# Kernel tuning notes

Measured on AMD Instinct MI355X. Metric: run time of the kernel, lower is better.

The kernel has to match this reference:

```python
import jax, jax.numpy as jnp
import numpy as np

EMBED_DIM = 1024
SEQ_LEN = 2048
BATCH = 8


def setup_inputs() -> dict:
    key = jax.random.key(0)
    ks = jax.random.split(key, 7)
    s = 1.0 / np.sqrt(EMBED_DIM)
    x = jax.random.normal(ks[0], (BATCH, SEQ_LEN, EMBED_DIM), dtype=jnp.float32)
    # torch nn.Linear stores weight as [out, in]; init U(-1/sqrt(in), 1/sqrt(in))
    Wq = jax.random.uniform(ks[1], (EMBED_DIM, EMBED_DIM), jnp.float32, -s, s)
    bq = jax.random.uniform(ks[2], (EMBED_DIM,), jnp.float32, -s, s)
    Wk = jax.random.uniform(ks[3], (EMBED_DIM, EMBED_DIM), jnp.float32, -s, s)
    bk = jax.random.uniform(ks[4], (EMBED_DIM,), jnp.float32, -s, s)
    Wv = jax.random.uniform(ks[5], (EMBED_DIM, EMBED_DIM), jnp.float32, -s, s)
    bv = jax.random.uniform(ks[6], (EMBED_DIM,), jnp.float32, -s, s)
    return {"x": x, "Wq": Wq, "bq": bq, "Wk": Wk, "bk": bk, "Wv": Wv, "bv": bv}


def reference(x, Wq, bq, Wk, bk, Wv, bv):
    # Linear projections (torch Linear: x @ W.T + b)
    q = jnp.einsum("bse,oe->bso", x, Wq) + bq
    k = jnp.einsum("bse,oe->bso", x, Wk) + bk
    v = jnp.einsum("bse,oe->bso", x, Wv) + bv
    scale = 1.0 / jnp.sqrt(jnp.float32(EMBED_DIM))
    sims = jnp.einsum("bqe,bke->bqk", q, k) * scale  # [B, S, S]
    causal = jnp.tril(jnp.ones((SEQ_LEN, SEQ_LEN), dtype=bool))
    masked = jnp.where(causal, sims, jnp.float32(-1e9))
    attn = jax.nn.softmax(masked, axis=2)
    return jnp.einsum("bqk,bke->bqe", attn, v)
```

## Files before the change

kernel.cpp:

```cpp
#include <hip/hip_runtime.h>
#include <hip/hip_bf16.h>
#include <stdint.h>
#include <math.h>

#define DEVI __device__ __forceinline__

typedef __attribute__((ext_vector_type(8))) __bf16    bf16x8;
typedef __attribute__((ext_vector_type(8))) _Float16  f16x8;
typedef __attribute__((ext_vector_type(4))) float     f32x4;

constexpr int BM = 128, BN = 128, BK = 64;

DEVI unsigned int pack2(float a, float b) {
  unsigned short ha = __builtin_bit_cast(unsigned short, __float2bfloat16(a));
  unsigned short hb = __builtin_bit_cast(unsigned short, __float2bfloat16(b));
  return (unsigned int)ha | ((unsigned int)hb << 16);
}

__global__ __launch_bounds__(256) void k_cvt_all(const float* __restrict__ x,
                                                 const float* __restrict__ Wq,
                                                 const float* __restrict__ Wk,
                                                 const float* __restrict__ Wv,
                                                 __hip_bfloat16* __restrict__ xb,
                                                 __hip_bfloat16* __restrict__ Wqb,
                                                 __hip_bfloat16* __restrict__ Wkb,
                                                 __hip_bfloat16* __restrict__ Wvb) {
  int i = blockIdx.x * 256 + threadIdx.x;
  const float* src;
  __hip_bfloat16* dst;
  int k;
  if (i < 4194304) {
    src = x; dst = xb; k = i;
  } else {
    int j = i - 4194304;
    int w = j >> 18;
    k = j & 262143;
    src = (w == 0) ? Wq : (w == 1) ? Wk : Wv;
    dst = (w == 0) ? Wqb : (w == 1) ? Wkb : Wvb;
  }
  float4 f = ((const float4*)src)[k];
  uint2 u;
  u.x = pack2(f.x, f.y);
  u.y = pack2(f.z, f.w);
  ((uint2*)dst)[k] = u;
}

DEVI void stage_tile(const __hip_bfloat16* gbase, int ld, unsigned short* lds, int tid) {
#pragma unroll
  for (int j = 0; j < 4; ++j) {
    int g   = j * 256 + tid;
    int row = g >> 3;
    int cp  = g & 7;
    int c   = cp ^ (row & 7);
    const __hip_bfloat16* src = gbase + (size_t)row * ld + c * 8;
    unsigned short* dst = lds + (size_t)(j * 256 + (tid & ~63)) * 8;
    __builtin_amdgcn_global_load_lds((__attribute__((address_space(1))) void*)(src),
                                     (__attribute__((address_space(3))) void*)(dst),
                                     16, 0, 0);
  }
}

DEVI bf16x8 read_frag(const unsigned short* lds, int row, int kcol) {
  int c  = kcol >> 3;
  int cp = c ^ (row & 7);
  return *(const bf16x8*)(lds + row * 64 + cp * 8);
}

DEVI void gemm_core(const __hip_bfloat16* A0, int lda,
                    const __hip_bfloat16* B0, int ldb,
                    int ktiles, f32x4 (&acc)[4][4]) {
  __shared__ unsigned short sA[BM * BK];
  __shared__ unsigned short sB[BN * BK];
  const int tid  = threadIdx.x;
  const int lane = tid & 63;
  const int wid  = tid >> 6;
  const int quad = lane >> 4;
  const int lr   = lane & 15;
  const int wm   = (wid >> 1) * 64;
  const int wn   = (wid & 1) * 64;
  const f32x4 Z = {0.f, 0.f, 0.f, 0.f};
#pragma unroll
  for (int i = 0; i < 4; ++i)
#pragma unroll
    for (int j = 0; j < 4; ++j) acc[i][j] = Z;

  for (int kt = 0; kt < ktiles; ++kt) {
    stage_tile(A0 + kt * BK, lda, sA, tid);
    stage_tile(B0 + kt * BK, ldb, sB, tid);
    __syncthreads();
#pragma unroll
    for (int ks = 0; ks < BK; ks += 32) {
      bf16x8 af[4], bfr[4];
#pragma unroll
      for (int t = 0; t < 4; ++t) af[t]  = read_frag(sA, wm + t * 16 + lr, ks + quad * 8);
#pragma unroll
      for (int t = 0; t < 4; ++t) bfr[t] = read_frag(sB, wn + t * 16 + lr, ks + quad * 8);
#pragma unroll
      for (int i = 0; i < 4; ++i)
#pragma unroll
        for (int j = 0; j < 4; ++j)
          acc[i][j] = __builtin_amdgcn_mfma_f32_16x16x32_bf16(af[i], bfr[j], acc[i][j], 0, 0, 0);
    }
    __syncthreads();
  }
}

__global__ __launch_bounds__(256, 4) void k_proj_qkv(const __hip_bfloat16* __restrict__ X,
                                                     const __hip_bfloat16* __restrict__ Wq,
                                                     const __hip_bfloat16* __restrict__ Wk,
                                                     const __hip_bfloat16* __restrict__ Wv,
                                                     const float* __restrict__ bq,
                                                     const float* __restrict__ bk,
                                                     const float* __restrict__ bv,
                                                     __hip_bfloat16* __restrict__ Q,
                                                     __hip_bfloat16* __restrict__ Kp,
                                                     __hip_bfloat16* __restrict__ Vt) {
  const int id = blockIdx.x;
  const int w  = id >> 10;
  const int i2 = id & 1023;
  const int mt = ((i2 & 7) << 4) | ((i2 >> 3) & 15);
  const int nt = i2 >> 7;
  const int m0 = mt * BM;
  const int n0 = nt * BN;

  const __hip_bfloat16* W = (w == 0) ? Wq : (w == 1) ? Wk : Wv;
  const float* bias       = (w == 0) ? bq : (w == 1) ? bk : bv;

  f32x4 acc[4][4];
  gemm_core(X + (size_t)m0 * 1024, 1024, W + (size_t)n0 * 1024, 1024, 16, acc);

  const int tid = threadIdx.x, lane = tid & 63, wid = tid >> 6;
  const int quad = lane >> 4, lr = lane & 15;
  const int wm = (wid >> 1) * 64, wn = (wid & 1) * 64;
  float bvv[4];
#pragma unroll
  for (int j = 0; j < 4; ++j) bvv[j] = bias[n0 + wn + j * 16 + lr];

  if (w != 2) {
    __hip_bfloat16* C = (w == 0) ? Q : Kp;
#pragma unroll
    for (int i = 0; i < 4; ++i)
#pragma unroll
      for (int j = 0; j < 4; ++j) {
        int n = n0 + wn + j * 16 + lr;
#pragma unroll
        for (int r = 0; r < 4; ++r) {
          int m = m0 + wm + i * 16 + quad * 4 + r;
          C[(size_t)m * 1024 + n] = __float2bfloat16(acc[i][j][r] + bvv[j]);
        }
      }
  } else {
    const int b = m0 >> 11;
    __hip_bfloat16* Cb = Vt + ((size_t)b << 21);
    const int sb = (m0 & 2047) + wm;
#pragma unroll
    for (int i = 0; i < 4; ++i)
#pragma unroll
      for (int j = 0; j < 4; ++j) {
        int n  = n0 + wn + j * 16 + lr;
        int s0 = sb + i * 16 + quad * 4;
        uint2 u;
        u.x = pack2(acc[i][j][0] + bvv[j], acc[i][j][1] + bvv[j]);
        u.y = pack2(acc[i][j][2] + bvv[j], acc[i][j][3] + bvv[j]);
        *(uint2*)(Cb + (size_t)n * 2048 + s0) = u;
      }
  }
}

__global__ __launch_bounds__(256, 4) void k_scores(const __hip_bfloat16* __restrict__ Q,
                                                   const __hip_bfloat16* __restrict__ Kmat,
                                                   _Float16* __restrict__ S, int b0) {
  const int id = blockIdx.x;
  const int z = id & 3;
  const int b = b0 + z;
  const int i = id >> 2;
  int qt = (int)((sqrtf(8.f * (float)i + 1.f) - 1.f) * 0.5f);
  while ((qt + 1) * (qt + 2) / 2 <= i) ++qt;
  while (qt * (qt + 1) / 2 > i) --qt;
  const int kt = i - qt * (qt + 1) / 2;

  const int m0 = qt * BM, n0 = kt * BN;
  f32x4 acc[4][4];
  const __hip_bfloat16* A0 = Q    + ((size_t)b << 21) + (size_t)m0 * 1024;
  const __hip_bfloat16* B0 = Kmat + ((size_t)b << 21) + (size_t)n0 * 1024;
  gemm_core(A0, 1024, B0, 1024, 16, acc);

  _Float16* Sb = S + ((size_t)z << 22);
  const int tid = threadIdx.x, lane = tid & 63, wid = tid >> 6;
  const int quad = lane >> 4, lr = lane & 15;
  const int wm = (wid >> 1) * 64, wn = (wid & 1) * 64;
#pragma unroll
  for (int i2 = 0; i2 < 4; ++i2)
#pragma unroll
    for (int j = 0; j < 4; ++j) {
      int n = n0 + wn + j * 16 + lr;
#pragma unroll
      for (int r = 0; r < 4; ++r) {
        int m = m0 + wm + i2 * 16 + quad * 4 + r;
        Sb[(size_t)m * 2048 + n] = (_Float16)(acc[i2][j][r] * 0.03125f);
      }
    }
}

__global__ __launch_bounds__(256) void k_softmax(_Float16* __restrict__ S) {
  const int row = blockIdx.x;
  const int q = row & 2047;
  _Float16* srow = S + ((size_t)row << 11);
  const int t = threadIdx.x;
  const int k0 = t << 3;

  f16x8 h = ((const f16x8*)srow)[t];
  float v[8];
  float mx = -1e30f;
#pragma unroll
  for (int i = 0; i < 8; ++i) {
    float f = (float)h[i];
    v[i] = (k0 + i <= q) ? f : -1e30f;
    mx = fmaxf(mx, v[i]);
  }
#pragma unroll
  for (int off = 32; off > 0; off >>= 1) mx = fmaxf(mx, __shfl_xor(mx, off));
  __shared__ float rmax[4], rsum[4];
  if ((t & 63) == 0) rmax[t >> 6] = mx;
  __syncthreads();
  mx = fmaxf(fmaxf(rmax[0], rmax[1]), fmaxf(rmax[2], rmax[3]));

  float e[8], s = 0.f;
#pragma unroll
  for (int i = 0; i < 8; ++i) { e[i] = __expf(v[i] - mx); s += e[i]; }
#pragma unroll
  for (int off = 32; off > 0; off >>= 1) s += __shfl_xor(s, off);
  if ((t & 63) == 0) rsum[t >> 6] = s;
  __syncthreads();
  s = rsum[0] + rsum[1] + rsum[2] + rsum[3];
  const float inv = 1.0f / s;

  bf16x8 o;
#pragma unroll
  for (int i = 0; i < 8; ++i) o[i] = (__bf16)(e[i] * inv);
  ((bf16x8*)srow)[t] = o;
}

__global__ __launch_bounds__(256, 4) void k_pv(const _Float16* __restrict__ Sbase,
                                               const __hip_bfloat16* __restrict__ Vt,
                                               float* __restrict__ out, int b0) {
  const int id = blockIdx.x;
  const int z = id & 3;
  const int b = b0 + z;
  const int r2 = id >> 2;
  const int nt = r2 & 7;
  const int qt = 15 - (r2 >> 3);
  const int m0 = qt * BM, n0 = nt * BN;
  const __hip_bfloat16* P  = (const __hip_bfloat16*)(Sbase + ((size_t)z << 22));
  const __hip_bfloat16* A0 = P + (size_t)m0 * 2048;
  const __hip_bfloat16* B0 = Vt + ((size_t)b << 21) + (size_t)n0 * 2048;
  const int ktiles = 2 * qt + 2;
  f32x4 acc[4][4];
  gemm_core(A0, 2048, B0, 2048, ktiles, acc);

  float* Cb = out + ((size_t)b << 21);
  const int tid = threadIdx.x, lane = tid & 63, wid = tid >> 6;
  const int quad = lane >> 4, lr = lane & 15;
  const int wm = (wid >> 1) * 64, wn = (wid & 1) * 64;
#pragma unroll
  for (int i = 0; i < 4; ++i)
#pragma unroll
    for (int j = 0; j < 4; ++j) {
      int n = n0 + wn + j * 16 + lr;
#pragma unroll
      for (int r = 0; r < 4; ++r) {
        int m = m0 + wm + i * 16 + quad * 4 + r;
        Cb[(size_t)m * 1024 + n] = acc[i][j][r];
      }
    }
}

extern "C" void kernel_launch(void* const* d_in, const int* in_sizes, int n_in,
                              void* d_out, int out_size, void* d_ws, size_t ws_size,
                              hipStream_t stream) {
  const float* x  = (const float*)d_in[0];
  const float* Wq = (const float*)d_in[1];
  const float* bq = (const float*)d_in[2];
  const float* Wk = (const float*)d_in[3];
  const float* bk = (const float*)d_in[4];
  const float* Wv = (const float*)d_in[5];
  const float* bv = (const float*)d_in[6];
  float* out = (float*)d_out;

  char* ws = (char*)d_ws;
  const size_t MB32 = (size_t)33554432;
  __hip_bfloat16* xb  = (__hip_bfloat16*)(ws);
  __hip_bfloat16* Wqb = (__hip_bfloat16*)(ws + MB32);
  __hip_bfloat16* Wkb = (__hip_bfloat16*)(ws + MB32 + 2097152);
  __hip_bfloat16* Wvb = (__hip_bfloat16*)(ws + MB32 + 4194304);
  __hip_bfloat16* Q   = (__hip_bfloat16*)(ws + MB32 + 6291456);
  __hip_bfloat16* Kp  = (__hip_bfloat16*)(ws + 2 * MB32 + 6291456);
  __hip_bfloat16* Vt  = (__hip_bfloat16*)(ws + 3 * MB32 + 6291456);
  _Float16*       S   = (_Float16*)(ws);

  dim3 blk(256);
  k_cvt_all<<<dim3(19456), blk, 0, stream>>>(x, Wq, Wk, Wv, xb, Wqb, Wkb, Wvb);
  k_proj_qkv<<<dim3(3072), blk, 0, stream>>>(xb, Wqb, Wkb, Wvb, bq, bk, bv, Q, Kp, Vt);

  const int G = 4;
  for (int b0 = 0; b0 < 8; b0 += G) {
    k_scores <<<dim3(G * 136),  blk, 0, stream>>>(Q, Kp, S, b0);
    k_softmax<<<dim3(G * 2048), blk, 0, stream>>>(S);
    k_pv     <<<dim3(G * 128),  blk, 0, stream>>>(S, Vt, out, b0);
  }
}
```

Before: 369.9 us.

## Pair causal PV tiles per block, batch all 8 heads when workspace allows, skip masked loads

The PV kernel now has each block process two query tiles (qt=15-p and qt=p), so every block does the same amount of causal work and the long-tail imbalance goes away. When the workspace is large enough, all 8 batches run in a single scores/softmax/PV pass instead of two groups, which cuts launches and gives larger grids. Softmax skips loading fully masked 8-element chunks. Shared buffers move into the kernels so the paired PV calls reuse them. The PV grid halves to 64 blocks per batch, which may lower occupancy, and the choice of path depends on the workspace size.

```diff
diff --git a/kernel.cpp b/kernel.cpp
--- a/kernel.cpp
+++ b/kernel.cpp
@@ -66,11 +66,10 @@
   return *(const bf16x8*)(lds + row * 64 + cp * 8);
 }
 
-DEVI void gemm_core(const __hip_bfloat16* A0, int lda,
+DEVI void gemm_core(unsigned short* sA, unsigned short* sB,
+                    const __hip_bfloat16* A0, int lda,
                     const __hip_bfloat16* B0, int ldb,
                     int ktiles, f32x4 (&acc)[4][4]) {
-  __shared__ unsigned short sA[BM * BK];
-  __shared__ unsigned short sB[BN * BK];
   const int tid  = threadIdx.x;
   const int lane = tid & 63;
   const int wid  = tid >> 6;
@@ -115,6 +114,8 @@
                                                      __hip_bfloat16* __restrict__ Q,
                                                      __hip_bfloat16* __restrict__ Kp,
                                                      __hip_bfloat16* __restrict__ Vt) {
+  __shared__ unsigned short sA[BM * BK];
+  __shared__ unsigned short sB[BN * BK];
   const int id = blockIdx.x;
   const int w  = id >> 10;
   const int i2 = id & 1023;
@@ -127,7 +128,7 @@
   const float* bias       = (w == 0) ? bq : (w == 1) ? bk : bv;
 
   f32x4 acc[4][4];
-  gemm_core(X + (size_t)m0 * 1024, 1024, W + (size_t)n0 * 1024, 1024, 16, acc);
+  gemm_core(sA, sB, X + (size_t)m0 * 1024, 1024, W + (size_t)n0 * 1024, 1024, 16, acc);
 
   const int tid = threadIdx.x, lane = tid & 63, wid = tid >> 6;
   const int quad = lane >> 4, lr = lane & 15;
@@ -169,11 +170,14 @@
 
 __global__ __launch_bounds__(256, 4) void k_scores(const __hip_bfloat16* __restrict__ Q,
                                                    const __hip_bfloat16* __restrict__ Kmat,
-                                                   _Float16* __restrict__ S, int b0) {
+                                                   _Float16* __restrict__ S,
+                                                   int b0, int zmask, int zshift) {
+  __shared__ unsigned short sA[BM * BK];
+  __shared__ unsigned short sB[BN * BK];
   const int id = blockIdx.x;
-  const int z = id & 3;
+  const int z = id & zmask;
   const int b = b0 + z;
-  const int i = id >> 2;
+  const int i = id >> zshift;
   int qt = (int)((sqrtf(8.f * (float)i + 1.f) - 1.f) * 0.5f);
   while ((qt + 1) * (qt + 2) / 2 <= i) ++qt;
   while (qt * (qt + 1) / 2 > i) --qt;
@@ -183,7 +187,7 @@
   f32x4 acc[4][4];
   const __hip_bfloat16* A0 = Q    + ((size_t)b << 21) + (size_t)m0 * 1024;
   const __hip_bfloat16* B0 = Kmat + ((size_t)b << 21) + (size_t)n0 * 1024;
-  gemm_core(A0, 1024, B0, 1024, 16, acc);
+  gemm_core(sA, sB, A0, 1024, B0, 1024, 16, acc);
 
   _Float16* Sb = S + ((size_t)z << 22);
   const int tid = threadIdx.x, lane = tid & 63, wid = tid >> 6;
@@ -209,14 +213,19 @@
   const int t = threadIdx.x;
   const int k0 = t << 3;
 
-  f16x8 h = ((const f16x8*)srow)[t];
   float v[8];
   float mx = -1e30f;
-#pragma unroll
-  for (int i = 0; i < 8; ++i) {
-    float f = (float)h[i];
-    v[i] = (k0 + i <= q) ? f : -1e30f;
-    mx = fmaxf(mx, v[i]);
+  if (k0 <= q) {
+    f16x8 h = ((const f16x8*)srow)[t];
+#pragma unroll
+    for (int i = 0; i < 8; ++i) {
+      float f = (float)h[i];
+      v[i] = (k0 + i <= q) ? f : -1e30f;
+      mx = fmaxf(mx, v[i]);
+    }
+  } else {
+#pragma unroll
+    for (int i = 0; i < 8; ++i) v[i] = -1e30f;
   }
 #pragma unroll
   for (int off = 32; off > 0; off >>= 1) mx = fmaxf(mx, __shfl_xor(mx, off));
@@ -241,24 +250,14 @@
   ((bf16x8*)srow)[t] = o;
 }
 
-__global__ __launch_bounds__(256, 4) void k_pv(const _Float16* __restrict__ Sbase,
-                                               const __hip_bfloat16* __restrict__ Vt,
-                                               float* __restrict__ out, int b0) {
-  const int id = blockIdx.x;
-  const int z = id & 3;
-  const int b = b0 + z;
-  const int r2 = id >> 2;
-  const int nt = r2 & 7;
-  const int qt = 15 - (r2 >> 3);
+DEVI void pv_one(unsigned short* sA, unsigned short* sB,
+                 const __hip_bfloat16* P, const __hip_bfloat16* VtB,
+                 float* Cb, int qt, int nt) {
   const int m0 = qt * BM, n0 = nt * BN;
-  const __hip_bfloat16* P  = (const __hip_bfloat16*)(Sbase + ((size_t)z << 22));
-  const __hip_bfloat16* A0 = P + (size_t)m0 * 2048;
-  const __hip_bfloat16* B0 = Vt + ((size_t)b << 21) + (size_t)n0 * 2048;
   const int ktiles = 2 * qt + 2;
   f32x4 acc[4][4];
-  gemm_core(A0, 2048, B0, 2048, ktiles, acc);
-
-  float* Cb = out + ((size_t)b << 21);
+  gemm_core(sA, sB, P + (size_t)m0 * 2048, 2048, VtB + (size_t)n0 * 2048, 2048, ktiles, acc);
+
   const int tid = threadIdx.x, lane = tid & 63, wid = tid >> 6;
   const int quad = lane >> 4, lr = lane & 15;
   const int wm = (wid >> 1) * 64, wn = (wid & 1) * 64;
@@ -273,6 +272,25 @@
         Cb[(size_t)m * 1024 + n] = acc[i][j][r];
       }
     }
+}
+
+__global__ __launch_bounds__(256, 4) void k_pv(const _Float16* __restrict__ Sbase,
+                                               const __hip_bfloat16* __restrict__ Vt,
+                                               float* __restrict__ out,
+                                               int b0, int zmask, int zshift) {
+  __shared__ unsigned short sA[BM * BK];
+  __shared__ unsigned short sB[BN * BK];
+  const int id = blockIdx.x;
+  const int z = id & zmask;
+  const int b = b0 + z;
+  const int r2 = id >> zshift;
+  const int nt = r2 & 7;
+  const int p  = (r2 >> 3) & 7;
+  const __hip_bfloat16* P   = (const __hip_bfloat16*)(Sbase + ((size_t)z << 22));
+  const __hip_bfloat16* VtB = Vt + ((size_t)b << 21);
+  float* Cb = out + ((size_t)b << 21);
+  pv_one(sA, sB, P, VtB, Cb, 15 - p, nt);
+  pv_one(sA, sB, P, VtB, Cb, p, nt);
 }
 
 extern "C" void kernel_launch(void* const* d_in, const int* in_sizes, int n_in,
@@ -289,23 +307,42 @@
 
   char* ws = (char*)d_ws;
   const size_t MB32 = (size_t)33554432;
-  __hip_bfloat16* xb  = (__hip_bfloat16*)(ws);
-  __hip_bfloat16* Wqb = (__hip_bfloat16*)(ws + MB32);
-  __hip_bfloat16* Wkb = (__hip_bfloat16*)(ws + MB32 + 2097152);
-  __hip_bfloat16* Wvb = (__hip_bfloat16*)(ws + MB32 + 4194304);
-  __hip_bfloat16* Q   = (__hip_bfloat16*)(ws + MB32 + 6291456);
-  __hip_bfloat16* Kp  = (__hip_bfloat16*)(ws + 2 * MB32 + 6291456);
-  __hip_bfloat16* Vt  = (__hip_bfloat16*)(ws + 3 * MB32 + 6291456);
-  _Float16*       S   = (_Float16*)(ws);
+  const size_t MB64 = (size_t)67108864;
+
+  __hip_bfloat16 *xb, *Wqb, *Wkb, *Wvb, *Q, *Kp, *Vt;
+  _Float16* S;
+  int G;
+  if (ws_size >= (size_t)174063616) {
+    S   = (_Float16*)(ws);
+    xb  = (__hip_bfloat16*)(ws);
+    Wqb = (__hip_bfloat16*)(ws + MB64);
+    Wkb = (__hip_bfloat16*)(ws + MB64 + 2097152);
+    Wvb = (__hip_bfloat16*)(ws + MB64 + 4194304);
+    Q   = (__hip_bfloat16*)(ws + MB64 + 6291456);
+    Kp  = (__hip_bfloat16*)(ws + MB64 + 6291456 + MB32);
+    Vt  = (__hip_bfloat16*)(ws + MB64 + 6291456 + 2 * MB32);
+    G = 8;
+  } else {
+    S   = (_Float16*)(ws);
+    xb  = (__hip_bfloat16*)(ws);
+    Wqb = (__hip_bfloat16*)(ws + MB32);
+    Wkb = (__hip_bfloat16*)(ws + MB32 + 2097152);
+    Wvb = (__hip_bfloat16*)(ws + MB32 + 4194304);
+    Q   = (__hip_bfloat16*)(ws + MB32 + 6291456);
+    Kp  = (__hip_bfloat16*)(ws + 2 * MB32 + 6291456);
+    Vt  = (__hip_bfloat16*)(ws + 3 * MB32 + 6291456);
+    G = 4;
+  }
+  const int zmask  = G - 1;
+  const int zshift = (G == 8) ? 3 : 2;
 
   dim3 blk(256);
   k_cvt_all<<<dim3(19456), blk, 0, stream>>>(x, Wq, Wk, Wv, xb, Wqb, Wkb, Wvb);
   k_proj_qkv<<<dim3(3072), blk, 0, stream>>>(xb, Wqb, Wkb, Wvb, bq, bk, bv, Q, Kp, Vt);
 
-  const int G = 4;
   for (int b0 = 0; b0 < 8; b0 += G) {
-    k_scores <<<dim3(G * 136),  blk, 0, stream>>>(Q, Kp, S, b0);
+    k_scores <<<dim3(G * 136),  blk, 0, stream>>>(Q, Kp, S, b0, zmask, zshift);
     k_softmax<<<dim3(G * 2048), blk, 0, stream>>>(S);
-    k_pv     <<<dim3(G * 128),  blk, 0, stream>>>(S, Vt, out, b0);
-  }
-}
+    k_pv     <<<dim3(G * 64),   blk, 0, stream>>>(S, Vt, out, b0, zmask, zshift);
+  }
+}
```

After: 344.9 us. 1.07x faster.
